# Optimization experiments

Hardware: AMD Instinct MI355X
Metric: run time of the kernel (lower is better)

## Reference

```python
import jax, jax.numpy as jnp
import numpy as np

B, S, D, H = 2, 2048, 1024, 16
HD = D // H  # 64
MASK_VAL = -10000.0


def setup_inputs() -> dict:
    key = jax.random.key(0)
    ks = jax.random.split(key, 8)
    sc = 0.02
    q_features = jax.random.normal(ks[0], (B, S, D), jnp.float32)
    kv_features = jax.random.normal(ks[1], (B, S, D), jnp.float32)
    # causal mask, broadcastable (1,1,S,S)
    mask = jnp.tril(jnp.ones((S, S), jnp.bool_))[None, None]
    Wq = jax.random.normal(ks[2], (D, D), jnp.float32) * sc
    bq = jnp.zeros((D,), jnp.float32)
    Wkv = jax.random.normal(ks[3], (D, 2 * D), jnp.float32) * sc
    bkv = jnp.zeros((2 * D,), jnp.float32)
    Wp = jax.random.normal(ks[4], (D, D), jnp.float32) * sc
    bp = jnp.zeros((D,), jnp.float32)
    return {"q_features": q_features, "kv_features": kv_features, "mask": mask,
            "Wq": Wq, "bq": bq, "Wkv": Wkv, "bkv": bkv, "Wp": Wp, "bp": bp}


def _split_heads(t):
    # (B,S,D) -> (B,H,S,HD)
    return t.reshape(B, S, H, HD).transpose(0, 2, 1, 3)


def reference(q_features, kv_features, mask, Wq, bq, Wkv, bkv, Wp, bp):
    query = q_features @ Wq + bq            # (B,S,D)
    kv = kv_features @ Wkv + bkv            # (B,S,2D)
    key, value = jnp.split(kv, 2, axis=-1)
    q = _split_heads(query)                 # (B,H,S,HD)
    k = _split_heads(key)
    v = _split_heads(value)
    scores = jnp.einsum('bhqd,bhkd->bhqk', q, k) / jnp.sqrt(jnp.float32(HD))
    scores = jnp.where(mask, scores, jnp.asarray(MASK_VAL, scores.dtype))
    attn = jax.nn.softmax(scores, axis=-1)  # (B,H,S,S)
    out = jnp.einsum('bhqk,bhkd->bhqd', attn, v)
    out = out.transpose(0, 2, 1, 3).reshape(B, S, D)  # merge heads
    return out @ Wp + bp
```

## Files before the change

kernel.cpp:

```cpp
#include <hip/hip_runtime.h>

typedef unsigned short u16;
typedef unsigned int u32;
typedef __attribute__((ext_vector_type(4))) unsigned short us4;
typedef __attribute__((ext_vector_type(8))) unsigned short us8;
typedef __attribute__((ext_vector_type(4))) short s16x4;
typedef __attribute__((ext_vector_type(8))) __bf16 bf16x8;
typedef __attribute__((ext_vector_type(4))) float floatx4;

#define S_ 2048
#define D_ 1024
#define QSC 0.18033688f

__device__ __forceinline__ float b2f(u16 u) {
  unsigned v = ((unsigned)u) << 16;
  return __builtin_bit_cast(float, v);
}
__device__ __forceinline__ u16 f2bf(float f) {
  unsigned u = __builtin_bit_cast(unsigned, f);
  unsigned r = (u + 0x7fffu + ((u >> 16) & 1u)) >> 16;
  return (u16)r;
}
__device__ __forceinline__ u16 f2bf_rhu(float f) {
  return (u16)((__builtin_bit_cast(unsigned, f) + 0x8000u) >> 16);
}

typedef const __attribute__((address_space(1))) u32* gas_t;
typedef __attribute__((address_space(3))) u32* las_t;
__device__ __forceinline__ void gload16(const u16* g, u16* l) {
  __builtin_amdgcn_global_load_lds((gas_t)g, (las_t)l, 16, 0, 0);
}

#define PBAR()                                   \
  {                                              \
    __builtin_amdgcn_sched_barrier(0);           \
    asm volatile("" ::: "memory");               \
    __builtin_amdgcn_s_barrier();                \
    asm volatile("" ::: "memory");               \
    __builtin_amdgcn_sched_barrier(0);           \
  }
#define WAITVM(N) asm volatile("s_waitcnt vmcnt(" #N ")" ::: "memory")

__global__ __launch_bounds__(256) void prep(
    const float* __restrict__ qf, const float* __restrict__ kvf,
    const float* __restrict__ Wq, const float* __restrict__ Wkv,
    const float* __restrict__ Wp, u16* __restrict__ qa, u16* __restrict__ kva,
    u16* __restrict__ Wqt, u16* __restrict__ Wkvt, u16* __restrict__ Wpt) {
  int bid = blockIdx.x, tid = threadIdx.x;
  if (bid < 4096) {
    const float* src = (bid < 2048) ? qf : kvf;
    u16* dst = (bid < 2048) ? qa : kva;
    size_t i = ((size_t)(bid & 2047) * 256 + tid) * 8;
    floatx4 a = *(const floatx4*)(src + i);
    floatx4 b = *(const floatx4*)(src + i + 4);
    us8 r;
#pragma unroll
    for (int j = 0; j < 4; j++) { r[j] = f2bf(a[j]); r[4 + j] = f2bf(b[j]); }
    *(us8*)(dst + i) = r;
  } else {
    int t = bid - 4096;
    const float* src; u16* dst; int R, C;
    if (t < 1024)      { src = Wq;  dst = Wqt;  R = 1024; C = 1024; }
    else if (t < 3072) { t -= 1024; src = Wkv; dst = Wkvt; R = 1024; C = 2048; }
    else               { t -= 3072; src = Wp;  dst = Wpt;  R = 1024; C = 1024; }
    int bx = t % (C >> 5), by = t / (C >> 5);
    __shared__ u16 tile[32][33];
    int tx = tid & 31, ty = tid >> 5;
    int x = bx * 32 + tx;
    for (int i = ty; i < 32; i += 8)
      tile[i][tx] = f2bf(src[(size_t)(by * 32 + i) * C + x]);
    __syncthreads();
    int ox = by * 32 + tx;
    for (int i = ty; i < 32; i += 8)
      dst[(size_t)(bx * 32 + i) * R + ox] = tile[tx][i];
  }
}

template <int MODE>
__device__ __forceinline__ void gemm256(
    const u16* __restrict__ A, const u16* __restrict__ Bt,
    const float* __restrict__ bias, void* __restrict__ C0,
    u16* __restrict__ C1, int N, int m0, int n0, u16* smem, float cscale) {
  int tid = threadIdx.x;
  int w = tid >> 6, lane = tid & 63;
  int quad = lane >> 4, l16 = lane & 15;
  int wr = w >> 2, wc = w & 3;

  int srow = w * 32 + (lane >> 2);
  int gchunk = ((lane & 3) ^ ((lane >> 3) & 3)) << 3;
  const u16* Asrc = A + (size_t)(m0 + srow) * 1024 + gchunk;
  const u16* Bsrc = Bt + (size_t)(n0 + srow) * 1024 + gchunk;
  u16* Adst = smem + w * 1024;
  u16* Bdst = smem + 32768 + w * 1024;

  int swz = (quad ^ ((l16 >> 1) & 3)) << 3;
  int aoff = (wr * 128 + l16) * 32 + swz;
  int boff = 32768 + (wc * 64 + l16) * 32 + swz;

  floatx4 acc[8][4] = {};

#define STAGE_A(t)                                             \
  {                                                            \
    int s_ = (t) & 3;                                          \
    gload16(Asrc + (t) * 32, Adst + s_ * 8192);                \
    gload16(Asrc + (t) * 32 + 16384, Adst + s_ * 8192 + 512);  \
  }
#define STAGE_B(t)                                             \
  {                                                            \
    int s_ = (t) & 3;                                          \
    gload16(Bsrc + (t) * 32, Bdst + s_ * 8192);                \
    gload16(Bsrc + (t) * 32 + 16384, Bdst + s_ * 8192 + 512);  \
  }

  STAGE_A(0); STAGE_B(0); STAGE_A(1); STAGE_B(1); STAGE_A(2); STAGE_B(2);
  WAITVM(8);
  PBAR();

  bf16x8 af[4], bf[4];

#define PHASE_A(t, DOSTAGE)                                                 \
  {                                                                         \
    int s_ = (t) & 3;                                                       \
    _Pragma("unroll") for (int mf = 0; mf < 4; mf++)                        \
        af[mf] = __builtin_bit_cast(                                        \
            bf16x8, *(const us8*)&smem[s_ * 8192 + aoff + mf * 512]);       \
    _Pragma("unroll") for (int nf = 0; nf < 4; nf++)                        \
        bf[nf] = __builtin_bit_cast(                                        \
            bf16x8, *(const us8*)&smem[s_ * 8192 + boff + nf * 512]);       \
    if (DOSTAGE) STAGE_A((t) + 3);                                          \
    PBAR();                                                                 \
    __builtin_amdgcn_s_setprio(1);                                          \
    _Pragma("unroll") for (int mf = 0; mf < 4; mf++)                        \
        _Pragma("unroll") for (int nf = 0; nf < 4; nf++)                    \
            acc[mf][nf] = __builtin_amdgcn_mfma_f32_16x16x32_bf16(          \
                af[mf], bf[nf], acc[mf][nf], 0, 0, 0);                      \
    __builtin_amdgcn_s_setprio(0);                                          \
    PBAR();                                                                 \
  }
#define PHASE_B(t, DOSTAGE, VMW)                                            \
  {                                                                         \
    int s_ = (t) & 3;                                                       \
    _Pragma("unroll") for (int mf = 0; mf < 4; mf++)                        \
        af[mf] = __builtin_bit_cast(                                        \
            bf16x8,                                                         \
            *(const us8*)&smem[s_ * 8192 + aoff + 2048 + mf * 512]);        \
    if (DOSTAGE) STAGE_B((t) + 3);                                          \
    PBAR();                                                                 \
    __builtin_amdgcn_s_setprio(1);                                          \
    _Pragma("unroll") for (int mf = 0; mf < 4; mf++)                        \
        _Pragma("unroll") for (int nf = 0; nf < 4; nf++)                    \
            acc[4 + mf][nf] = __builtin_amdgcn_mfma_f32_16x16x32_bf16(      \
                af[mf], bf[nf], acc[4 + mf][nf], 0, 0, 0);                  \
    __builtin_amdgcn_s_setprio(0);                                          \
    VMW;                                                                    \
    PBAR();                                                                 \
  }

#pragma unroll 1
  for (int t = 0; t < 29; t++) {
    PHASE_A(t, true);
    PHASE_B(t, true, WAITVM(4));
  }
  PHASE_A(29, false); PHASE_B(29, false, (void)0);
  PHASE_A(30, false); PHASE_B(30, false, WAITVM(0));
  PHASE_A(31, false); PHASE_B(31, false, (void)0);

#undef PHASE_A
#undef PHASE_B
#undef STAGE_A
#undef STAGE_B

#pragma unroll
  for (int mf = 0; mf < 8; mf++) {
#pragma unroll
    for (int nf = 0; nf < 4; nf++) {
      int col = n0 + wc * 64 + nf * 16 + l16;
      int rowq = m0 + wr * 128 + mf * 16 + quad * 4;
      float bv = bias[col];
      if (MODE == 0) {
        u16* o = (u16*)C0;
#pragma unroll
        for (int r = 0; r < 4; r++)
          o[(size_t)(rowq + r) * N + col] = f2bf((acc[mf][nf][r] + bv) * cscale);
      } else {
        if (col < 1024) {
          u16* o = (u16*)C0;
#pragma unroll
          for (int r = 0; r < 4; r++)
            o[(size_t)(rowq + r) * 1024 + col] = f2bf(acc[mf][nf][r] + bv);
        } else {
          int vcol = col - 1024;
          int b = rowq >> 11, s0 = rowq & 2047;
          us4 pv;
#pragma unroll
          for (int r = 0; r < 4; r++) pv[r] = f2bf(acc[mf][nf][r] + bv);
          *(us4*)&C1[((size_t)(b * 1024 + vcol)) * (size_t)S_ + s0] = pv;
        }
      }
    }
  }
}

__global__ __launch_bounds__(512, 2) void gemm_qkv(
    const u16* __restrict__ qa, const u16* __restrict__ kva,
    const u16* __restrict__ Wqt, const u16* __restrict__ Wkvt,
    const float* __restrict__ bq, const float* __restrict__ bkv,
    u16* __restrict__ Qb, u16* __restrict__ Kb, u16* __restrict__ Vt) {
  __shared__ __align__(16) u16 smem[65536];
  int bid = blockIdx.x;
  if (bid < 64) {
    gemm256<0>(qa, Wqt, bq, Qb, nullptr, 1024,
               (bid >> 2) * 256, (bid & 3) * 256, smem, QSC);
  } else {
    int lb = bid - 64;
    gemm256<2>(kva, Wkvt, bkv, Kb, Vt, 2048,
               (lb >> 3) * 256, (lb & 7) * 256, smem, 1.0f);
  }
}

template <int TM, int TN, int MODE>
__device__ __forceinline__ void gemm_core(
    const u16* __restrict__ A, const u16* __restrict__ Bt,
    const float* __restrict__ bias, void* __restrict__ C0,
    u16* __restrict__ C1, int N, int n0, int m0,
    u16* As, u16* Bs, float cscale) {
  constexpr int MT = TM / 32, NT = TN / 32;
  int tid  = threadIdx.x;
  int wave = tid >> 6, lane = tid & 63;
  int quad = lane >> 4, l16 = lane & 15;
  int wr = wave >> 1, wc = wave & 1;
  const u16* Ag = A  + (size_t)(m0 + wave * 8 + (lane >> 3)) * 1024 + (lane & 7) * 8;
  const u16* Bg = Bt + (size_t)(n0 + wave * 8 + (lane >> 3)) * 1024 + (lane & 7) * 8;
  u16* Aw = As + wave * 8 * 64;
  u16* Bw = Bs + wave * 8 * 64;
  floatx4 acc[MT][NT] = {};
  for (int k0 = 0; k0 < 1024; k0 += 64) {
    if (k0) __syncthreads();
#pragma unroll
    for (int p = 0; p < TM / 32; p++)
      gload16(Ag + (size_t)p * 32 * 1024 + k0, Aw + p * 32 * 64);
#pragma unroll
    for (int p = 0; p < TN / 32; p++)
      gload16(Bg + (size_t)p * 32 * 1024 + k0, Bw + p * 32 * 64);
    __syncthreads();
#pragma unroll
    for (int kk = 0; kk < 2; kk++) {
      bf16x8 af[MT], bf[NT];
#pragma unroll
      for (int mt = 0; mt < MT; mt++)
        af[mt] = __builtin_bit_cast(bf16x8,
            *(const us8*)&As[(wr * (TM / 2) + mt * 16 + l16) * 64 + (kk * 4 + quad) * 8]);
#pragma unroll
      for (int nt = 0; nt < NT; nt++)
        bf[nt] = __builtin_bit_cast(bf16x8,
            *(const us8*)&Bs[(wc * (TN / 2) + nt * 16 + l16) * 64 + (kk * 4 + quad) * 8]);
#pragma unroll
      for (int mt = 0; mt < MT; mt++)
#pragma unroll
        for (int nt = 0; nt < NT; nt++)
          acc[mt][nt] = __builtin_amdgcn_mfma_f32_16x16x32_bf16(
              af[mt], bf[nt], acc[mt][nt], 0, 0, 0);
    }
  }
#pragma unroll
  for (int mt = 0; mt < MT; mt++) {
#pragma unroll
    for (int nt = 0; nt < NT; nt++) {
      int col  = n0 + wc * (TN / 2) + nt * 16 + l16;
      int rowq = m0 + wr * (TM / 2) + mt * 16 + quad * 4;
      float bv = bias[col];
      if (MODE == 0) {
        u16* o = (u16*)C0;
#pragma unroll
        for (int r = 0; r < 4; r++)
          o[(size_t)(rowq + r) * N + col] = f2bf((acc[mt][nt][r] + bv) * cscale);
      } else if (MODE == 1) {
        float* o = (float*)C0;
#pragma unroll
        for (int r = 0; r < 4; r++)
          o[(size_t)(rowq + r) * N + col] = acc[mt][nt][r] + bv;
      } else {
        if (col < 1024) {
          u16* o = (u16*)C0;
#pragma unroll
          for (int r = 0; r < 4; r++)
            o[(size_t)(rowq + r) * 1024 + col] = f2bf(acc[mt][nt][r] + bv);
        } else {
          int vcol = col - 1024;
          int b = rowq >> 11, s0 = rowq & 2047;
          us4 pv;
#pragma unroll
          for (int r = 0; r < 4; r++) pv[r] = f2bf(acc[mt][nt][r] + bv);
          *(us4*)&C1[((size_t)(b * 1024 + vcol)) * (size_t)S_ + s0] = pv;
        }
      }
    }
  }
}

__global__ __launch_bounds__(256) void gemm_out(
    const u16* __restrict__ AO, const u16* __restrict__ Wpt,
    const float* __restrict__ bp, float* __restrict__ out) {
  __shared__ __align__(16) u16 As[64 * 64];
  __shared__ __align__(16) u16 Bs[128 * 64];
  gemm_core<64, 128, 1>(AO, Wpt, bp, out, nullptr, 1024,
                        (blockIdx.x & 7) * 128, (blockIdx.x >> 3) * 64, As, Bs, 1.0f);
}

__global__ __launch_bounds__(512) void attn_fwd(
    const u16* __restrict__ Q, const u16* __restrict__ Kb,
    const u16* __restrict__ Vt, u16* __restrict__ O,
    u16* __restrict__ Opart, float* __restrict__ ml) {
  __shared__ __align__(16) u16 sm[16384];
  int tid  = threadIdx.x;
  int w    = tid >> 6, lane = tid & 63;
  int quad = lane >> 4, l16 = lane & 15;
  int bh = blockIdx.x, b = bh >> 4, h = bh & 15;
  int y = blockIdx.y;

  static const signed char yt_[24] = {15,15,7,14,14,13,13,6,12,12,11,11,5,
                                      10,10,9,9,4,8,8,3,2,1,0};
  static const signed char yh_[24] = {0,1,-1,0,1,0,1,-1,0,1,0,1,-1,
                                      0,1,0,1,-1,0,1,-1,-1,-1,-1};
  int t = yt_[y], hh = yh_[y];
  bool split = hh >= 0;
  int kb0, kb1;
  if (split) { kb0 = hh ? (t + 1) : 0; kb1 = hh ? (2 * t + 2) : (t + 1); }
  else       { kb0 = 0; kb1 = 2 * t + 2; }
  int n = kb1 - kb0;

  const size_t row0 = (size_t)b * S_;
  const u16* Kg = Kb + row0 * D_ + h * 64;
  const u16* Vg = Vt + ((size_t)b * 1024 + h * 64) * S_;

  int qlo = t * 128 + w * 16;
  int dkb = qlo >> 6;
  int qg  = (qlo & 63) + l16;

  const u16* qp = Q + (row0 + qlo + l16) * D_ + h * 64 + quad * 8;
  bf16x8 aqv[2];
  aqv[0] = __builtin_bit_cast(bf16x8, *(const us8*)(qp));
  aqv[1] = __builtin_bit_cast(bf16x8, *(const us8*)(qp + 32));

  floatx4 o_[4] = {};
  floatx4 l_acc = {};
  const s16x4 ones4 = {0x3F80, 0x3F80, 0x3F80, 0x3F80};

  int srow = tid >> 3, c8 = tid & 7;
  int woff = srow * 64 + ((c8 ^ (srow & 7)) << 3);
  u16* smK = sm;
  u16* smV = sm + 8192;

  const u16* Kp = Kg + (size_t)(kb0 * 64 + srow) * D_ + c8 * 8;
  const u16* Vp = Vg + (size_t)srow * S_ + kb0 * 64 + c8 * 8;
  us8 pk = *(const us8*)Kp, pv = *(const us8*)Vp;
  *(us8*)&smK[woff] = pk;
  *(us8*)&smV[woff] = pv;
  if (n > 1) {
    Kp += (size_t)64 * D_; Vp += 64;
    pk = *(const us8*)Kp; pv = *(const us8*)Vp;
  }
  __syncthreads();

  for (int i = 0; i < n; i++) {
    int cur = i & 1;
    int kb = kb0 + i;
    if (i + 1 < n) {
      int nxt = (cur ^ 1) * 4096;
      *(us8*)&smK[nxt + woff] = pk;
      *(us8*)&smV[nxt + woff] = pv;
      if (i + 2 < n) {
        Kp += (size_t)64 * D_; Vp += 64;
        pk = *(const us8*)Kp; pv = *(const us8*)Vp;
      }
    }
    if (kb <= dkb) {
      const u16* Ksb = smK + cur * 4096;
      const u16* Vsb = smV + cur * 4096;

      floatx4 s[4] = {};
      __builtin_amdgcn_s_setprio(1);
#pragma unroll
      for (int kk = 0; kk < 2; kk++)
#pragma unroll
        for (int nt = 0; nt < 4; nt++) {
          us8 kf = *(const us8*)&Ksb[(nt * 16 + l16) * 64 +
                                     (((kk * 4 + quad) ^ (l16 & 7)) << 3)];
          s[nt] = __builtin_amdgcn_mfma_f32_16x16x32_bf16(
              __builtin_bit_cast(bf16x8, kf), aqv[kk], s[nt], 0, 0, 0);
        }
      __builtin_amdgcn_s_setprio(0);

      if (kb == dkb) {
#pragma unroll
        for (int nt = 0; nt < 4; nt++)
#pragma unroll
          for (int r = 0; r < 4; r++)
            if (nt * 16 + quad * 4 + r > qg) s[nt][r] = -1e5f;
      }

      s16x4 pb[4];
#pragma unroll
      for (int nt = 0; nt < 4; nt++)
#pragma unroll
        for (int r = 0; r < 4; r++)
          pb[nt][r] = (short)f2bf_rhu(__builtin_amdgcn_exp2f(s[nt][r]));

      __builtin_amdgcn_s_setprio(1);
#pragma unroll
      for (int nt = 0; nt < 4; nt++) {
        l_acc = __builtin_amdgcn_mfma_f32_16x16x16bf16_1k(ones4, pb[nt], l_acc, 0, 0, 0);
#pragma unroll
        for (int mt = 0; mt < 4; mt++) {
          int hd = mt * 16 + l16;
          int chunk = nt * 2 + (quad >> 1);
          us4 vf = *(const us4*)&Vsb[hd * 64 + ((chunk ^ (l16 & 7)) << 3) + (quad & 1) * 4];
          o_[mt] = __builtin_amdgcn_mfma_f32_16x16x16bf16_1k(
              __builtin_bit_cast(s16x4, vf), pb[nt], o_[mt], 0, 0, 0);
        }
      }
      __builtin_amdgcn_s_setprio(0);
    }
    __syncthreads();
  }

  if (!split) {
    float rl = __builtin_amdgcn_rcpf(l_acc[0]);
    size_t orow = (row0 + qlo + l16) * D_ + h * 64;
#pragma unroll
    for (int mt = 0; mt < 4; mt++) {
      us4 ov;
#pragma unroll
      for (int r = 0; r < 4; r++) ov[r] = f2bf(o_[mt][r] * rl);
      *(us4*)&O[orow + mt * 16 + quad * 4] = ov;
    }
  } else {
    int part = (t - 8) * 2 + hh;
    u16* op = Opart + ((size_t)(bh * 16 + part)) * 8192;
    int rloc = w * 16 + l16;
#pragma unroll
    for (int mt = 0; mt < 4; mt++) {
      us4 ov;
#pragma unroll
      for (int r = 0; r < 4; r++) ov[r] = f2bf(o_[mt][r]);
      *(us4*)&op[rloc * 64 + mt * 16 + quad * 4] = ov;
    }
    if (quad == 0)
      ml[(size_t)(bh * 16 + part) * 128 + rloc] = l_acc[0];
  }
}

__global__ __launch_bounds__(256) void combine(
    const u16* __restrict__ Opart, const float* __restrict__ ml,
    u16* __restrict__ O) {
  int bh = blockIdx.x, b = bh >> 4, h = bh & 15;
  int t = 8 + blockIdx.y;
  int p0 = bh * 16 + (t - 8) * 2;
  const u16* o1 = Opart + (size_t)p0 * 8192;
  const u16* o2 = o1 + 8192;
  int row = threadIdx.x >> 1, ch = (threadIdx.x & 1) * 32;
  float l1 = ml[(size_t)p0 * 128 + row];
  float l2 = ml[(size_t)(p0 + 1) * 128 + row];
  float inv = __builtin_amdgcn_rcpf(l1 + l2);
  size_t orow = ((size_t)b * S_ + t * 128 + row) * D_ + h * 64 + ch;
#pragma unroll
  for (int v = 0; v < 4; v++) {
    us8 x1 = *(const us8*)&o1[row * 64 + ch + v * 8];
    us8 x2 = *(const us8*)&o2[row * 64 + ch + v * 8];
    us8 out;
#pragma unroll
    for (int j = 0; j < 8; j++)
      out[j] = f2bf((b2f(x1[j]) + b2f(x2[j])) * inv);
    *(us8*)&O[orow + v * 8] = out;
  }
}

extern "C" void kernel_launch(void* const* d_in, const int* in_sizes, int n_in,
                              void* d_out, int out_size, void* d_ws, size_t ws_size,
                              hipStream_t stream) {
  const float* qf  = (const float*)d_in[0];
  const float* kvf = (const float*)d_in[1];
  const float* Wq  = (const float*)d_in[3];
  const float* bq  = (const float*)d_in[4];
  const float* Wkv = (const float*)d_in[5];
  const float* bkv = (const float*)d_in[6];
  const float* Wp  = (const float*)d_in[7];
  const float* bp  = (const float*)d_in[8];

  char* ws = (char*)d_ws;
  const size_t MB = 1048576;
  u16*   kva  = (u16*)(ws);
  u16*   AO   = (u16*)(ws);
  u16*   Kbp  = (u16*)(ws + 8 * MB);
  u16*   Vtp  = (u16*)(ws + 16 * MB);
  u16*   Wqt  = (u16*)(ws + 24 * MB);
  float* mlp  = (float*)(ws + 24 * MB);
  u16*   Wkvt = (u16*)(ws + 26 * MB);
  u16*   Wpt  = (u16*)(ws + 30 * MB);
  u16*   qa    = (u16*)d_out;
  u16*   Opart = (u16*)d_out;
  u16*   Qb    = (u16*)d_out + (size_t)4 * 1048576;

  prep<<<8192, 256, 0, stream>>>(qf, kvf, Wq, Wkv, Wp, qa, kva, Wqt, Wkvt, Wpt);
  gemm_qkv<<<192, 512, 0, stream>>>(qa, kva, Wqt, Wkvt, bq, bkv, Qb, Kbp, Vtp);
  attn_fwd<<<dim3(32, 24), 512, 0, stream>>>(Qb, Kbp, Vtp, AO, Opart, mlp);
  combine<<<dim3(32, 8), 256, 0, stream>>>(Opart, mlp, AO);
  gemm_out<<<512, 256, 0, stream>>>(AO, Wpt, bp, (float*)d_out);
}
```

Baseline: 214.8 us.

## Restructure QKV GEMM to double-buffered BK=64 pipeline and remap blocks across XCDs

```diff
diff --git a/kernel.cpp b/kernel.cpp
--- a/kernel.cpp
+++ b/kernel.cpp
@@ -86,89 +86,64 @@
   int quad = lane >> 4, l16 = lane & 15;
   int wr = w >> 2, wc = w & 3;
 
-  int srow = w * 32 + (lane >> 2);
-  int gchunk = ((lane & 3) ^ ((lane >> 3) & 3)) << 3;
-  const u16* Asrc = A + (size_t)(m0 + srow) * 1024 + gchunk;
-  const u16* Bsrc = Bt + (size_t)(n0 + srow) * 1024 + gchunk;
-  u16* Adst = smem + w * 1024;
-  u16* Bdst = smem + 32768 + w * 1024;
-
-  int swz = (quad ^ ((l16 >> 1) & 3)) << 3;
-  int aoff = (wr * 128 + l16) * 32 + swz;
-  int boff = 32768 + (wc * 64 + l16) * 32 + swz;
+  int gch = ((lane & 7) ^ ((lane >> 3) & 7)) << 3;
+  const u16* Ag = A + (size_t)(m0 + w * 32 + (lane >> 3)) * 1024 + gch;
+  const u16* Bg = Bt + (size_t)(n0 + w * 32 + (lane >> 3)) * 1024 + gch;
+  u16* Adst = smem + w * 32 * 64;
+  u16* Bdst = smem + 32768 + w * 32 * 64;
+
+  int ab = (wr * 128 + l16) * 64;
+  int bb = 32768 + (wc * 64 + l16) * 64;
+  int xk0 = (quad ^ (l16 & 7)) << 3;
+  int xk1 = ((4 + quad) ^ (l16 & 7)) << 3;
 
   floatx4 acc[8][4] = {};
 
-#define STAGE_A(t)                                             \
-  {                                                            \
-    int s_ = (t) & 3;                                          \
-    gload16(Asrc + (t) * 32, Adst + s_ * 8192);                \
-    gload16(Asrc + (t) * 32 + 16384, Adst + s_ * 8192 + 512);  \
-  }
-#define STAGE_B(t)                                             \
-  {                                                            \
-    int s_ = (t) & 3;                                          \
-    gload16(Bsrc + (t) * 32, Bdst + s_ * 8192);                \
-    gload16(Bsrc + (t) * 32 + 16384, Bdst + s_ * 8192 + 512);  \
-  }
-
-  STAGE_A(0); STAGE_B(0); STAGE_A(1); STAGE_B(1); STAGE_A(2); STAGE_B(2);
-  WAITVM(8);
+#define STAGE3(tn, SD)                                                  \
+  {                                                                     \
+    _Pragma("unroll") for (int i = 0; i < 4; i++) {                     \
+      gload16(Ag + (size_t)(tn) * 64 + (size_t)i * 8192,                \
+              Adst + (SD) + i * 512);                                   \
+      gload16(Bg + (size_t)(tn) * 64 + (size_t)i * 8192,                \
+              Bdst + (SD) + i * 512);                                   \
+    }                                                                   \
+  }
+
+#define COMPUTE3(SOFF)                                                  \
+  {                                                                     \
+    _Pragma("unroll") for (int kk = 0; kk < 2; kk++) {                  \
+      int xk = kk ? xk1 : xk0;                                          \
+      bf16x8 bfr[4];                                                    \
+      _Pragma("unroll") for (int nf = 0; nf < 4; nf++)                  \
+        bfr[nf] = __builtin_bit_cast(bf16x8,                            \
+            *(const us8*)&smem[(SOFF) + bb + nf * 1024 + xk]);          \
+      _Pragma("unroll") for (int mf = 0; mf < 8; mf++) {                \
+        bf16x8 afr = __builtin_bit_cast(bf16x8,                         \
+            *(const us8*)&smem[(SOFF) + ab + mf * 1024 + xk]);          \
+        _Pragma("unroll") for (int nf = 0; nf < 4; nf++)                \
+          acc[mf][nf] = __builtin_amdgcn_mfma_f32_16x16x32_bf16(        \
+              afr, bfr[nf], acc[mf][nf], 0, 0, 0);                      \
+      }                                                                 \
+    }                                                                   \
+  }
+
+  STAGE3(0, 0);
+  WAITVM(0);
   PBAR();
-
-  bf16x8 af[4], bf[4];
-
-#define PHASE_A(t, DOSTAGE)                                                 \
-  {                                                                         \
-    int s_ = (t) & 3;                                                       \
-    _Pragma("unroll") for (int mf = 0; mf < 4; mf++)                        \
-        af[mf] = __builtin_bit_cast(                                        \
-            bf16x8, *(const us8*)&smem[s_ * 8192 + aoff + mf * 512]);       \
-    _Pragma("unroll") for (int nf = 0; nf < 4; nf++)                        \
-        bf[nf] = __builtin_bit_cast(                                        \
-            bf16x8, *(const us8*)&smem[s_ * 8192 + boff + nf * 512]);       \
-    if (DOSTAGE) STAGE_A((t) + 3);                                          \
-    PBAR();                                                                 \
-    __builtin_amdgcn_s_setprio(1);                                          \
-    _Pragma("unroll") for (int mf = 0; mf < 4; mf++)                        \
-        _Pragma("unroll") for (int nf = 0; nf < 4; nf++)                    \
-            acc[mf][nf] = __builtin_amdgcn_mfma_f32_16x16x32_bf16(          \
-                af[mf], bf[nf], acc[mf][nf], 0, 0, 0);                      \
-    __builtin_amdgcn_s_setprio(0);                                          \
-    PBAR();                                                                 \
-  }
-#define PHASE_B(t, DOSTAGE, VMW)                                            \
-  {                                                                         \
-    int s_ = (t) & 3;                                                       \
-    _Pragma("unroll") for (int mf = 0; mf < 4; mf++)                        \
-        af[mf] = __builtin_bit_cast(                                        \
-            bf16x8,                                                         \
-            *(const us8*)&smem[s_ * 8192 + aoff + 2048 + mf * 512]);        \
-    if (DOSTAGE) STAGE_B((t) + 3);                                          \
-    PBAR();                                                                 \
-    __builtin_amdgcn_s_setprio(1);                                          \
-    _Pragma("unroll") for (int mf = 0; mf < 4; mf++)                        \
-        _Pragma("unroll") for (int nf = 0; nf < 4; nf++)                    \
-            acc[4 + mf][nf] = __builtin_amdgcn_mfma_f32_16x16x32_bf16(      \
-                af[mf], bf[nf], acc[4 + mf][nf], 0, 0, 0);                  \
-    __builtin_amdgcn_s_setprio(0);                                          \
-    VMW;                                                                    \
-    PBAR();                                                                 \
-  }
-
 #pragma unroll 1
-  for (int t = 0; t < 29; t++) {
-    PHASE_A(t, true);
-    PHASE_B(t, true, WAITVM(4));
-  }
-  PHASE_A(29, false); PHASE_B(29, false, (void)0);
-  PHASE_A(30, false); PHASE_B(30, false, WAITVM(0));
-  PHASE_A(31, false); PHASE_B(31, false, (void)0);
-
-#undef PHASE_A
-#undef PHASE_B
-#undef STAGE_A
-#undef STAGE_B
+  for (int t = 0; t < 16; t += 2) {
+    STAGE3(t + 1, 16384);
+    COMPUTE3(0);
+    WAITVM(0);
+    PBAR();
+    if (t + 2 < 16) STAGE3(t + 2, 0);
+    COMPUTE3(16384);
+    WAITVM(0);
+    PBAR();
+  }
+
+#undef STAGE3
+#undef COMPUTE3
 
 #pragma unroll
   for (int mf = 0; mf < 8; mf++) {
@@ -208,11 +183,12 @@
     u16* __restrict__ Qb, u16* __restrict__ Kb, u16* __restrict__ Vt) {
   __shared__ __align__(16) u16 smem[65536];
   int bid = blockIdx.x;
-  if (bid < 64) {
+  int work = (bid & 7) * 24 + (bid >> 3);
+  if (work < 64) {
     gemm256<0>(qa, Wqt, bq, Qb, nullptr, 1024,
-               (bid >> 2) * 256, (bid & 3) * 256, smem, QSC);
+               (work >> 2) * 256, (work & 3) * 256, smem, QSC);
   } else {
-    int lb = bid - 64;
+    int lb = work - 64;
     gemm256<2>(kva, Wkvt, bkv, Kb, Vt, 2048,
                (lb >> 3) * 256, (lb & 7) * 256, smem, 1.0f);
   }
@@ -303,8 +279,9 @@
     const float* __restrict__ bp, float* __restrict__ out) {
   __shared__ __align__(16) u16 As[64 * 64];
   __shared__ __align__(16) u16 Bs[128 * 64];
+  int work = (blockIdx.x & 7) * 64 + (blockIdx.x >> 3);
   gemm_core<64, 128, 1>(AO, Wpt, bp, out, nullptr, 1024,
-                        (blockIdx.x & 7) * 128, (blockIdx.x >> 3) * 64, As, Bs, 1.0f);
+                        (work & 7) * 128, (work >> 3) * 64, As, Bs, 1.0f);
 }
 
 __global__ __launch_bounds__(512) void attn_fwd(
```

Result: no change. 211.0 us (-1.8%).
